# Optimization experiments

Hardware: AMD Instinct MI355X
Metric: run time of the kernel (lower is better)

The kernel has to match this reference:

```python
import jax, jax.numpy as jnp
import numpy as np

N_NODES = 100000
N_EDGES = 1600000
VOCAB = 1000
EMB = 128
HID = 256
N_GRAPHS = 128
N_LABELS = 2


def setup_inputs() -> dict:
    key = jax.random.key(0)
    ks = jax.random.split(key, 16)
    s = 0.05
    inp = {
        "x_ids": jax.random.randint(ks[0], (N_NODES,), 0, VOCAB),
        "edge_index": jax.random.randint(ks[1], (2, N_EDGES), 0, N_NODES),
        "batch": jnp.sort(jax.random.randint(ks[2], (N_NODES,), 0, N_GRAPHS)),
        "emb": jax.random.normal(ks[3], (VOCAB, EMB)) * s,
        "W0": jax.random.normal(ks[4], (EMB, HID)) * s,
        "b0": jnp.zeros((HID,)),
        "W1": jax.random.normal(ks[5], (HID, HID)) * s,
        "b1": jnp.zeros((HID,)),
        "W2": jax.random.normal(ks[6], (HID, HID)) * s,
        "b2": jnp.zeros((HID,)),
        "W3": jax.random.normal(ks[7], (HID, HID)) * s,
        "b3": jnp.zeros((HID,)),
        "Wc1": jax.random.normal(ks[8], (2 * HID, HID)) * s,
        "bc1": jnp.zeros((HID,)),
        "Wc2": jax.random.normal(ks[9], (HID, N_LABELS)) * s,
        "bc2": jnp.zeros((N_LABELS,)),
    }
    return inp


def _gcn_conv(x, W, b, src, dst, dis):
    # GCNConv with self-loops: out = D^-1/2 (A+I) D^-1/2 (x W) + b
    xw = x @ W                                   # [N, H]
    norm = dis[src] * dis[dst]                   # [E]
    out = jnp.zeros_like(xw).at[dst].add(xw[src] * norm[:, None])
    out = out + xw * (dis * dis)[:, None]        # self-loop term
    return out + b


def reference(x_ids, edge_index, batch, emb, W0, b0, W1, b1, W2, b2, W3, b3,
              Wc1, bc1, Wc2, bc2):
    src, dst = edge_index[0], edge_index[1]
    # degree (incl. self loop) is the same every layer -> compute once
    deg = jnp.zeros((N_NODES,), jnp.float32).at[dst].add(1.0) + 1.0
    dis = jax.lax.rsqrt(deg)

    x = emb[x_ids]                               # [N, EMB]
    for W, b in ((W0, b0), (W1, b1), (W2, b2), (W3, b3)):
        x = jax.nn.relu(_gcn_conv(x, W, b, src, dst, dis))
        # dropout: identity in eval mode

    counts = jax.ops.segment_sum(jnp.ones((N_NODES,), x.dtype), batch,
                                 num_segments=N_GRAPHS)
    mean_pool = jax.ops.segment_sum(x, batch, num_segments=N_GRAPHS)
    mean_pool = mean_pool / jnp.maximum(counts, 1.0)[:, None]
    max_pool = jax.ops.segment_max(x, batch, num_segments=N_GRAPHS)
    max_pool = jnp.where(counts[:, None] > 0, max_pool, 0.0)

    g = jnp.concatenate([mean_pool, max_pool], axis=1)  # [G, 2H]
    h = jax.nn.relu(g @ Wc1 + bc1)
    logits = h @ Wc2 + bc2                               # [G, 2]
    return logits
```

## Files before the change

kernel.cpp:

```cpp
#include <hip/hip_runtime.h>
#include <hip/hip_bf16.h>
#include <cstdint>
#include <cstddef>

#define N_NODES 100000
#define N_EDGES 1600000
#define EMBD 128
#define HID 256
#define N_GRAPHS 128
#define VOCAB 1000
#define NB_SCAN 98

typedef short bf16x8 __attribute__((ext_vector_type(8)));
typedef float f32x4 __attribute__((ext_vector_type(4)));
typedef float f32x2 __attribute__((ext_vector_type(2)));

__device__ inline unsigned short rne_bf16(float f) {
  unsigned u = __float_as_uint(f);
  return (unsigned short)((u + 0x7FFFu + ((u >> 16) & 1u)) >> 16);
}
__device__ inline float bf16_to_f32(unsigned short h) {
  return __uint_as_float(((unsigned)h) << 16);
}
__device__ inline void split_hl(float v, unsigned short& h, unsigned short& l) {
  h = rne_bf16(v);
  float hf = __uint_as_float(((unsigned)h) << 16);
  l = rne_bf16(v - hf);
}
__device__ inline f32x4 cvt4(uint2 v) {
  f32x4 r;
  r[0] = __uint_as_float(v.x << 16);
  r[1] = __uint_as_float(v.x & 0xFFFF0000u);
  r[2] = __uint_as_float(v.y << 16);
  r[3] = __uint_as_float(v.y & 0xFFFF0000u);
  return r;
}
__device__ inline f32x2 cvt2(unsigned v) {
  f32x2 r;
  r[0] = __uint_as_float(v << 16);
  r[1] = __uint_as_float(v & 0xFFFF0000u);
  return r;
}

__global__ void k_indeg(const int* __restrict__ dst, int* __restrict__ indeg) {
  int e = blockIdx.x * 256 + threadIdx.x;
  if (e < N_EDGES) atomicAdd(&indeg[dst[e]], 1);
}

__global__ __launch_bounds__(1024)
void k_scan1(const int* __restrict__ indeg, int* __restrict__ off, int* __restrict__ bsum,
             float* __restrict__ dis) {
  __shared__ int s[1024];
  const int tid = threadIdx.x;
  int i = blockIdx.x * 1024 + tid;
  int v = (i < N_NODES) ? indeg[i] : 0;
  if (i < N_NODES) dis[i] = rsqrtf((float)(v + 1));
  s[tid] = v; __syncthreads();
  #pragma unroll
  for (int ofs = 1; ofs < 1024; ofs <<= 1) {
    int t2 = (tid >= ofs) ? s[tid - ofs] : 0;
    __syncthreads();
    s[tid] += t2;
    __syncthreads();
  }
  if (i < N_NODES) off[i] = s[tid] - v;
  if (tid == 1023) bsum[blockIdx.x] = s[1023];
}

__global__ void k_scan2(int* __restrict__ bsum) {
  if (threadIdx.x == 0) {
    int a = 0;
    for (int i = 0; i < NB_SCAN; ++i) { int t = bsum[i]; bsum[i] = a; a += t; }
    bsum[NB_SCAN] = a;
  }
}

__global__ __launch_bounds__(1024)
void k_scan3(int* __restrict__ off, int* __restrict__ cur, const int* __restrict__ bsum) {
  int i = blockIdx.x * 1024 + threadIdx.x;
  if (i < N_NODES) { int v = off[i] + bsum[blockIdx.x]; off[i] = v; cur[i] = v; }
  if (i == 0) off[N_NODES] = bsum[NB_SCAN];
}

__global__ void k_fill(const int* __restrict__ src, const int* __restrict__ dst,
                       const int* __restrict__ ids, const float* __restrict__ dis,
                       int* __restrict__ cursor, int2* __restrict__ csre,
                       int2* __restrict__ csre0) {
  int e = blockIdx.x * 256 + threadIdx.x;
  if (e < N_EDGES) {
    int s = src[e];
    float ds = dis[s];
    int p = atomicAdd(&cursor[dst[e]], 1);
    csre[p]  = make_int2(s, __float_as_int(ds));
    csre0[p] = make_int2(ids[s], __float_as_int(ds));
  }
}

__global__ void k_prep(const float* __restrict__ emb, unsigned short* __restrict__ emb16,
                       const float* __restrict__ W0, unsigned short* __restrict__ w0h,
                       unsigned short* __restrict__ w0l,
                       const float* __restrict__ W1, unsigned short* __restrict__ w1h,
                       unsigned short* __restrict__ w1l,
                       const float* __restrict__ W2, unsigned short* __restrict__ w2h,
                       unsigned short* __restrict__ w2l,
                       const float* __restrict__ W3, unsigned short* __restrict__ w3h,
                       unsigned short* __restrict__ w3l) {
  int i = blockIdx.x * 256 + threadIdx.x;
  if (i < VOCAB * EMBD) { emb16[i] = rne_bf16(emb[i]); return; }
  i -= VOCAB * EMBD;
  unsigned short h, l;
  if (i < EMBD * HID) {
    int k = i >> 8, n = i & 255;
    split_hl(W0[i], h, l);
    w0h[n * EMBD + k] = h; w0l[n * EMBD + k] = l;
    return;
  }
  i -= EMBD * HID;
  if (i >= 3 * HID * HID) return;
  int w = i >> 16, j = i & 65535;
  const float* Ws = (w == 0) ? W1 : (w == 1) ? W2 : W3;
  unsigned short* th = (w == 0) ? w1h : (w == 1) ? w2h : w3h;
  unsigned short* tl = (w == 0) ? w1l : (w == 1) ? w2l : w3l;
  int k = j >> 8, n = j & 255;
  split_hl(Ws[j], h, l);
  th[n * HID + k] = h; tl[n * HID + k] = l;
}

__global__ __launch_bounds__(256)
void k_agg0(const unsigned short* __restrict__ emb16, const int* __restrict__ ids,
            const float* __restrict__ dis, const int* __restrict__ off,
            const int2* __restrict__ csre0, unsigned short* __restrict__ aggA) {
  const int lane = threadIdx.x & 63;
  const int node = blockIdx.x * 4 + (threadIdx.x >> 6);
  const float di = dis[node];
  unsigned sv = *((const unsigned*)(emb16 + (size_t)ids[node] * EMBD) + lane);
  f32x2 a0 = di * cvt2(sv);
  f32x2 a1 = (f32x2)0.f, a2 = (f32x2)0.f, a3 = (f32x2)0.f;
  const int e0 = off[node], e1 = off[node + 1];
  int e = e0;
  for (; e + 4 <= e1; e += 4) {
    int2 c0 = csre0[e], c1 = csre0[e + 1], c2 = csre0[e + 2], c3 = csre0[e + 3];
    unsigned v0 = *((const unsigned*)(emb16 + (size_t)c0.x * EMBD) + lane);
    unsigned v1 = *((const unsigned*)(emb16 + (size_t)c1.x * EMBD) + lane);
    unsigned v2 = *((const unsigned*)(emb16 + (size_t)c2.x * EMBD) + lane);
    unsigned v3 = *((const unsigned*)(emb16 + (size_t)c3.x * EMBD) + lane);
    a0 += __int_as_float(c0.y) * cvt2(v0);
    a1 += __int_as_float(c1.y) * cvt2(v1);
    a2 += __int_as_float(c2.y) * cvt2(v2);
    a3 += __int_as_float(c3.y) * cvt2(v3);
  }
  for (; e < e1; ++e) {
    int2 c0 = csre0[e];
    unsigned v0 = *((const unsigned*)(emb16 + (size_t)c0.x * EMBD) + lane);
    a0 += __int_as_float(c0.y) * cvt2(v0);
  }
  f32x2 r = di * ((a0 + a1) + (a2 + a3));
  size_t base = (size_t)node * EMBD + lane * 2;
  *(ushort2*)&aggA[base] = make_ushort2(rne_bf16(r[0]), rne_bf16(r[1]));
}

__global__ __launch_bounds__(256)
void k_agg16(const unsigned short* __restrict__ y16, const float* __restrict__ dis,
             const int* __restrict__ off, const int2* __restrict__ csre,
             unsigned short* __restrict__ aggA) {
  const int lane = threadIdx.x & 63;
  const int node = blockIdx.x * 4 + (threadIdx.x >> 6);
  const float di = dis[node];
  uint2 sv = *((const uint2*)(y16 + (size_t)node * HID) + lane);
  f32x4 a0 = di * cvt4(sv);
  f32x4 a1 = (f32x4)0.f, a2 = (f32x4)0.f, a3 = (f32x4)0.f;
  const int e0 = off[node], e1 = off[node + 1];
  int e = e0;
  for (; e + 4 <= e1; e += 4) {
    int2 c0 = csre[e], c1 = csre[e + 1], c2 = csre[e + 2], c3 = csre[e + 3];
    uint2 v0 = *((const uint2*)(y16 + (size_t)c0.x * HID) + lane);
    uint2 v1 = *((const uint2*)(y16 + (size_t)c1.x * HID) + lane);
    uint2 v2 = *((const uint2*)(y16 + (size_t)c2.x * HID) + lane);
    uint2 v3 = *((const uint2*)(y16 + (size_t)c3.x * HID) + lane);
    a0 += __int_as_float(c0.y) * cvt4(v0);
    a1 += __int_as_float(c1.y) * cvt4(v1);
    a2 += __int_as_float(c2.y) * cvt4(v2);
    a3 += __int_as_float(c3.y) * cvt4(v3);
  }
  for (; e < e1; ++e) {
    int2 c0 = csre[e];
    uint2 v0 = *((const uint2*)(y16 + (size_t)c0.x * HID) + lane);
    a0 += __int_as_float(c0.y) * cvt4(v0);
  }
  f32x4 r = di * ((a0 + a1) + (a2 + a3));
  size_t base = (size_t)node * HID + lane * 4;
  *(ushort4*)&aggA[base] = make_ushort4(rne_bf16(r[0]), rne_bf16(r[1]),
                                        rne_bf16(r[2]), rne_bf16(r[3]));
}

template<int K>
__global__ __launch_bounds__(256)
void k_gemm_direct(const unsigned short* __restrict__ A,
                   const unsigned short* __restrict__ Wh, const unsigned short* __restrict__ Wl,
                   const float* __restrict__ bias, unsigned short* __restrict__ C16) {
  const int lane = threadIdx.x & 63;
  const int wid = threadIdx.x >> 6;
  const int wr = wid >> 1, wc = wid & 1;
  const int row0 = blockIdx.x * 128;
  const int col0 = blockIdx.y * 128;
  const int cl = lane & 15;
  const int sl = lane >> 4;

  int ra[4];
  #pragma unroll
  for (int f = 0; f < 4; ++f) {
    int r = row0 + wr * 64 + f * 16 + cl;
    ra[f] = (r < N_NODES) ? r : (N_NODES - 1);
  }
  const int cb = col0 + wc * 64 + cl;

  f32x4 acc[4][4];
  #pragma unroll
  for (int i = 0; i < 4; ++i)
    #pragma unroll
    for (int j = 0; j < 4; ++j) acc[i][j] = (f32x4)0.f;

  #pragma unroll
  for (int kt = 0; kt < K; kt += 32) {
    bf16x8 fa[4], fbh[4], fbl[4];
    #pragma unroll
    for (int f = 0; f < 4; ++f) {
      fa[f]  = *(const bf16x8*)&A [(size_t)ra[f] * K + kt + sl * 8];
      fbh[f] = *(const bf16x8*)&Wh[(size_t)(cb + f * 16) * K + kt + sl * 8];
      fbl[f] = *(const bf16x8*)&Wl[(size_t)(cb + f * 16) * K + kt + sl * 8];
    }
    #pragma unroll
    for (int i = 0; i < 4; ++i)
      #pragma unroll
      for (int j = 0; j < 4; ++j) {
        acc[i][j] = __builtin_amdgcn_mfma_f32_16x16x32_bf16(fa[i], fbh[j], acc[i][j], 0, 0, 0);
        acc[i][j] = __builtin_amdgcn_mfma_f32_16x16x32_bf16(fa[i], fbl[j], acc[i][j], 0, 0, 0);
      }
  }

  #pragma unroll
  for (int j = 0; j < 4; ++j) {
    int gn = col0 + wc * 64 + j * 16 + cl;
    float bn = bias[gn];
    #pragma unroll
    for (int i = 0; i < 4; ++i) {
      f32x4 v = acc[i][j];
      #pragma unroll
      for (int r = 0; r < 4; ++r) {
        int gm = row0 + wr * 64 + i * 16 + sl * 4 + r;
        if (gm < N_NODES) C16[(size_t)gm * HID + gn] = rne_bf16(fmaxf(v[r] + bn, 0.f));
      }
    }
  }
}

__device__ inline int lower_bound_i(const int* a, int n, int v) {
  int lo = 0, hi = n;
  while (lo < hi) { int m = (lo + hi) >> 1; if (a[m] < v) lo = m + 1; else hi = m; }
  return lo;
}

__global__ __launch_bounds__(256)
void k_pool(const unsigned short* __restrict__ y16, const int* __restrict__ batch,
            float* __restrict__ gsum, float* __restrict__ gmax) {
  const int gi = blockIdx.x, ck = blockIdx.y, t = threadIdx.x;
  const int start = lower_bound_i(batch, N_NODES, gi);
  const int end   = lower_bound_i(batch, N_NODES, gi + 1);
  const int len = end - start;
  const int c0 = start + (len * ck) / 4;
  const int c1 = start + (len * (ck + 1)) / 4;
  float sum = 0.f, mx = 0.f;
  #pragma unroll 4
  for (int n = c0; n < c1; ++n) {
    float v = bf16_to_f32(y16[(size_t)n * HID + t]);
    sum += v; mx = fmaxf(mx, v);
  }
  if (c0 < c1) {
    atomicAdd(&gsum[gi * HID + t], sum);
    atomicMax((int*)&gmax[gi * HID + t], __float_as_int(mx));
  }
}

__global__ __launch_bounds__(256)
void k_cls(const float* __restrict__ gsum, const float* __restrict__ gmax,
           const int* __restrict__ batch,
           const float* __restrict__ Wc1, const float* __restrict__ bc1,
           const float* __restrict__ Wc2, const float* __restrict__ bc2,
           float* __restrict__ out) {
  const int gi = blockIdx.x, t = threadIdx.x;
  __shared__ float sg[512];
  __shared__ float sh[256];
  const int start = lower_bound_i(batch, N_NODES, gi);
  const int end   = lower_bound_i(batch, N_NODES, gi + 1);
  const float rcnt = 1.f / (float)((end - start) > 0 ? (end - start) : 1);
  sg[t] = gsum[gi * HID + t] * rcnt;
  sg[256 + t] = gmax[gi * HID + t];
  __syncthreads();
  float a = bc1[t];
  #pragma unroll 8
  for (int k = 0; k < 512; ++k) a = fmaf(sg[k], Wc1[k * HID + t], a);
  sh[t] = fmaxf(a, 0.f);
  __syncthreads();
  if (t < 2) {
    float o = bc2[t];
    for (int k = 0; k < 256; ++k) o = fmaf(sh[k], Wc2[k * 2 + t], o);
    out[gi * 2 + t] = o;
  }
}

extern "C" void kernel_launch(void* const* d_in, const int* in_sizes, int n_in,
                              void* d_out, int out_size, void* d_ws, size_t ws_size,
                              hipStream_t stream) {
  const int*   x_ids = (const int*)d_in[0];
  const int*   ei    = (const int*)d_in[1];
  const int*   batch = (const int*)d_in[2];
  const float* emb   = (const float*)d_in[3];
  const float* W0 = (const float*)d_in[4];  const float* b0 = (const float*)d_in[5];
  const float* W1 = (const float*)d_in[6];  const float* b1 = (const float*)d_in[7];
  const float* W2 = (const float*)d_in[8];  const float* b2 = (const float*)d_in[9];
  const float* W3 = (const float*)d_in[10]; const float* b3 = (const float*)d_in[11];
  const float* Wc1 = (const float*)d_in[12]; const float* bc1 = (const float*)d_in[13];
  const float* Wc2 = (const float*)d_in[14]; const float* bc2 = (const float*)d_in[15];
  float* out = (float*)d_out;
  const int* src = ei;
  const int* dst = ei + N_EDGES;

  char* ws = (char*)d_ws;
  size_t o = 0;
  auto alloc = [&](size_t bytes) -> char* {
    char* p = ws + o; o += (bytes + 255) & ~(size_t)255; return p;
  };
  unsigned short* y16  = (unsigned short*)alloc((size_t)N_NODES * HID * 2);
  unsigned short* aggA = (unsigned short*)alloc((size_t)N_NODES * HID * 2);
  float* dis   = (float*)alloc((size_t)N_NODES * 4);
  int*   indeg = (int*)  alloc((size_t)N_NODES * 4);
  int*   off   = (int*)  alloc((size_t)(N_NODES + 1) * 4);
  int*   cur   = (int*)  alloc((size_t)(N_NODES + 1) * 4);
  int*   bsum  = (int*)  alloc((size_t)(NB_SCAN + 1) * 4);
  int2*  csre  = (int2*) alloc((size_t)N_EDGES * 8);
  int2*  csre0 = (int2*) alloc((size_t)N_EDGES * 8);
  unsigned short* emb16 = (unsigned short*)alloc((size_t)VOCAB * EMBD * 2);
  unsigned short* wbuf  = (unsigned short*)alloc((size_t)458752 * 2);
  float* gsum  = (float*)alloc((size_t)N_GRAPHS * HID * 4);
  float* gmax  = (float*)alloc((size_t)N_GRAPHS * HID * 4);
  (void)ws_size; (void)in_sizes; (void)n_in; (void)out_size;

  unsigned short* wt0h = wbuf;            unsigned short* wt0l = wbuf + 32768;
  unsigned short* wt1h = wbuf + 65536;    unsigned short* wt1l = wbuf + 131072;
  unsigned short* wt2h = wbuf + 196608;   unsigned short* wt2l = wbuf + 262144;
  unsigned short* wt3h = wbuf + 327680;   unsigned short* wt3l = wbuf + 393216;

  hipMemsetAsync(indeg, 0, (size_t)N_NODES * 4, stream);
  hipMemsetAsync(gsum, 0, (size_t)N_GRAPHS * HID * 4 * 2, stream);
  k_indeg<<<N_EDGES / 256, 256, 0, stream>>>(dst, indeg);
  k_scan1<<<NB_SCAN, 1024, 0, stream>>>(indeg, off, bsum, dis);
  k_scan2<<<1, 64, 0, stream>>>(bsum);
  k_scan3<<<NB_SCAN, 1024, 0, stream>>>(off, cur, bsum);
  k_fill<<<N_EDGES / 256, 256, 0, stream>>>(src, dst, x_ids, dis, cur, csre, csre0);
  k_prep<<<(VOCAB * EMBD + EMBD * HID + 3 * HID * HID + 255) / 256, 256, 0, stream>>>(
      emb, emb16, W0, wt0h, wt0l, W1, wt1h, wt1l, W2, wt2h, wt2l, W3, wt3h, wt3l);

  dim3 ggrid((N_NODES + 127) / 128, 2);
  k_agg0<<<N_NODES / 4, 256, 0, stream>>>(emb16, x_ids, dis, off, csre0, aggA);
  k_gemm_direct<128><<<ggrid, 256, 0, stream>>>(aggA, wt0h, wt0l, b0, y16);
  k_agg16<<<N_NODES / 4, 256, 0, stream>>>(y16, dis, off, csre, aggA);
  k_gemm_direct<256><<<ggrid, 256, 0, stream>>>(aggA, wt1h, wt1l, b1, y16);
  k_agg16<<<N_NODES / 4, 256, 0, stream>>>(y16, dis, off, csre, aggA);
  k_gemm_direct<256><<<ggrid, 256, 0, stream>>>(aggA, wt2h, wt2l, b2, y16);
  k_agg16<<<N_NODES / 4, 256, 0, stream>>>(y16, dis, off, csre, aggA);
  k_gemm_direct<256><<<ggrid, 256, 0, stream>>>(aggA, wt3h, wt3l, b3, y16);

  dim3 pgrid(N_GRAPHS, 4);
  k_pool<<<pgrid, 256, 0, stream>>>(y16, batch, gsum, gmax);
  k_cls<<<N_GRAPHS, 256, 0, stream>>>(gsum, gmax, batch, Wc1, bc1, Wc2, bc2, out);
}
```

Before: 1.079 ms.

## Fuse GCN neighbor aggregation into the GEMM via shared-memory row tiles

Each layer now runs one kernel: a block aggregates 64 node rows from the CSR into LDS as bf16, then does the split-bf16 MFMA GEMM across all 256 output columns with bias and ReLU, ping-ponging between two output buffers. This removes the global write and re-read of the aggregated activation matrix and halves kernel launches. In exchange each block runs its gather phase before its compute phase with only 4 waves, and the GEMM no longer tiles columns across blocks. The block-sum scan is also parallelised across 128 threads.

Result: slower. 1.289 ms (+19.4%).

```diff
diff --git a/kernel.cpp b/kernel.cpp
--- a/kernel.cpp
+++ b/kernel.cpp
@@ -68,11 +68,19 @@
 }
 
 __global__ void k_scan2(int* __restrict__ bsum) {
-  if (threadIdx.x == 0) {
-    int a = 0;
-    for (int i = 0; i < NB_SCAN; ++i) { int t = bsum[i]; bsum[i] = a; a += t; }
-    bsum[NB_SCAN] = a;
-  }
+  __shared__ int s[128];
+  const int t = threadIdx.x;
+  int v = (t < NB_SCAN) ? bsum[t] : 0;
+  s[t] = v; __syncthreads();
+  #pragma unroll
+  for (int ofs = 1; ofs < 128; ofs <<= 1) {
+    int x = (t >= ofs) ? s[t - ofs] : 0;
+    __syncthreads();
+    s[t] += x;
+    __syncthreads();
+  }
+  if (t < NB_SCAN) bsum[t] = s[t] - v;
+  if (t == 127) bsum[NB_SCAN] = s[127];
 }
 
 __global__ __launch_bounds__(1024)
@@ -126,108 +134,102 @@
   th[n * HID + k] = h; tl[n * HID + k] = l;
 }
 
-__global__ __launch_bounds__(256)
-void k_agg0(const unsigned short* __restrict__ emb16, const int* __restrict__ ids,
-            const float* __restrict__ dis, const int* __restrict__ off,
-            const int2* __restrict__ csre0, unsigned short* __restrict__ aggA) {
-  const int lane = threadIdx.x & 63;
-  const int node = blockIdx.x * 4 + (threadIdx.x >> 6);
-  const float di = dis[node];
-  unsigned sv = *((const unsigned*)(emb16 + (size_t)ids[node] * EMBD) + lane);
-  f32x2 a0 = di * cvt2(sv);
-  f32x2 a1 = (f32x2)0.f, a2 = (f32x2)0.f, a3 = (f32x2)0.f;
-  const int e0 = off[node], e1 = off[node + 1];
-  int e = e0;
-  for (; e + 4 <= e1; e += 4) {
-    int2 c0 = csre0[e], c1 = csre0[e + 1], c2 = csre0[e + 2], c3 = csre0[e + 3];
-    unsigned v0 = *((const unsigned*)(emb16 + (size_t)c0.x * EMBD) + lane);
-    unsigned v1 = *((const unsigned*)(emb16 + (size_t)c1.x * EMBD) + lane);
-    unsigned v2 = *((const unsigned*)(emb16 + (size_t)c2.x * EMBD) + lane);
-    unsigned v3 = *((const unsigned*)(emb16 + (size_t)c3.x * EMBD) + lane);
-    a0 += __int_as_float(c0.y) * cvt2(v0);
-    a1 += __int_as_float(c1.y) * cvt2(v1);
-    a2 += __int_as_float(c2.y) * cvt2(v2);
-    a3 += __int_as_float(c3.y) * cvt2(v3);
-  }
-  for (; e < e1; ++e) {
-    int2 c0 = csre0[e];
-    unsigned v0 = *((const unsigned*)(emb16 + (size_t)c0.x * EMBD) + lane);
-    a0 += __int_as_float(c0.y) * cvt2(v0);
-  }
-  f32x2 r = di * ((a0 + a1) + (a2 + a3));
-  size_t base = (size_t)node * EMBD + lane * 2;
-  *(ushort2*)&aggA[base] = make_ushort2(rne_bf16(r[0]), rne_bf16(r[1]));
-}
-
-__global__ __launch_bounds__(256)
-void k_agg16(const unsigned short* __restrict__ y16, const float* __restrict__ dis,
-             const int* __restrict__ off, const int2* __restrict__ csre,
-             unsigned short* __restrict__ aggA) {
-  const int lane = threadIdx.x & 63;
-  const int node = blockIdx.x * 4 + (threadIdx.x >> 6);
-  const float di = dis[node];
-  uint2 sv = *((const uint2*)(y16 + (size_t)node * HID) + lane);
-  f32x4 a0 = di * cvt4(sv);
-  f32x4 a1 = (f32x4)0.f, a2 = (f32x4)0.f, a3 = (f32x4)0.f;
-  const int e0 = off[node], e1 = off[node + 1];
-  int e = e0;
-  for (; e + 4 <= e1; e += 4) {
-    int2 c0 = csre[e], c1 = csre[e + 1], c2 = csre[e + 2], c3 = csre[e + 3];
-    uint2 v0 = *((const uint2*)(y16 + (size_t)c0.x * HID) + lane);
-    uint2 v1 = *((const uint2*)(y16 + (size_t)c1.x * HID) + lane);
-    uint2 v2 = *((const uint2*)(y16 + (size_t)c2.x * HID) + lane);
-    uint2 v3 = *((const uint2*)(y16 + (size_t)c3.x * HID) + lane);
-    a0 += __int_as_float(c0.y) * cvt4(v0);
-    a1 += __int_as_float(c1.y) * cvt4(v1);
-    a2 += __int_as_float(c2.y) * cvt4(v2);
-    a3 += __int_as_float(c3.y) * cvt4(v3);
-  }
-  for (; e < e1; ++e) {
-    int2 c0 = csre[e];
-    uint2 v0 = *((const uint2*)(y16 + (size_t)c0.x * HID) + lane);
-    a0 += __int_as_float(c0.y) * cvt4(v0);
-  }
-  f32x4 r = di * ((a0 + a1) + (a2 + a3));
-  size_t base = (size_t)node * HID + lane * 4;
-  *(ushort4*)&aggA[base] = make_ushort4(rne_bf16(r[0]), rne_bf16(r[1]),
-                                        rne_bf16(r[2]), rne_bf16(r[3]));
-}
-
 template<int K>
 __global__ __launch_bounds__(256)
-void k_gemm_direct(const unsigned short* __restrict__ A,
-                   const unsigned short* __restrict__ Wh, const unsigned short* __restrict__ Wl,
-                   const float* __restrict__ bias, unsigned short* __restrict__ C16) {
-  const int lane = threadIdx.x & 63;
-  const int wid = threadIdx.x >> 6;
-  const int wr = wid >> 1, wc = wid & 1;
-  const int row0 = blockIdx.x * 128;
-  const int col0 = blockIdx.y * 128;
+void k_fused(const unsigned short* __restrict__ xin, const int* __restrict__ ids,
+             const float* __restrict__ dis, const int* __restrict__ off,
+             const int2* __restrict__ csre,
+             const unsigned short* __restrict__ Wh, const unsigned short* __restrict__ Wl,
+             const float* __restrict__ bias, unsigned short* __restrict__ yout) {
+  constexpr int LDA = K + 8;
+  __shared__ unsigned short sA[64 * LDA];
+  const int tid = threadIdx.x;
+  const int lane = tid & 63;
+  const int wid = tid >> 6;
+  const int row0 = blockIdx.x * 64;
+
+  for (int n = 0; n < 16; ++n) {
+    const int lrow = wid * 16 + n;
+    const int node = row0 + lrow;
+    if constexpr (K == 256) {
+      f32x4 a0 = (f32x4)0.f, a1 = (f32x4)0.f, a2 = (f32x4)0.f, a3 = (f32x4)0.f;
+      if (node < N_NODES) {
+        const float di = dis[node];
+        uint2 sv = *((const uint2*)(xin + (size_t)node * 256) + lane);
+        a0 = di * cvt4(sv);
+        const int e0 = off[node], e1 = off[node + 1];
+        int e = e0;
+        for (; e + 4 <= e1; e += 4) {
+          int2 c0 = csre[e], c1 = csre[e + 1], c2 = csre[e + 2], c3 = csre[e + 3];
+          uint2 v0 = *((const uint2*)(xin + (size_t)c0.x * 256) + lane);
+          uint2 v1 = *((const uint2*)(xin + (size_t)c1.x * 256) + lane);
+          uint2 v2 = *((const uint2*)(xin + (size_t)c2.x * 256) + lane);
+          uint2 v3 = *((const uint2*)(xin + (size_t)c3.x * 256) + lane);
+          a0 += __int_as_float(c0.y) * cvt4(v0);
+          a1 += __int_as_float(c1.y) * cvt4(v1);
+          a2 += __int_as_float(c2.y) * cvt4(v2);
+          a3 += __int_as_float(c3.y) * cvt4(v3);
+        }
+        for (; e < e1; ++e) {
+          int2 c0 = csre[e];
+          uint2 v0 = *((const uint2*)(xin + (size_t)c0.x * 256) + lane);
+          a0 += __int_as_float(c0.y) * cvt4(v0);
+        }
+        f32x4 r = di * ((a0 + a1) + (a2 + a3));
+        *(ushort4*)&sA[lrow * LDA + lane * 4] =
+            make_ushort4(rne_bf16(r[0]), rne_bf16(r[1]), rne_bf16(r[2]), rne_bf16(r[3]));
+      } else {
+        *(ushort4*)&sA[lrow * LDA + lane * 4] = make_ushort4(0, 0, 0, 0);
+      }
+    } else {
+      f32x2 a0 = (f32x2)0.f, a1 = (f32x2)0.f, a2 = (f32x2)0.f, a3 = (f32x2)0.f;
+      if (node < N_NODES) {
+        const float di = dis[node];
+        unsigned sv = *((const unsigned*)(xin + (size_t)ids[node] * 128) + lane);
+        a0 = di * cvt2(sv);
+        const int e0 = off[node], e1 = off[node + 1];
+        int e = e0;
+        for (; e + 4 <= e1; e += 4) {
+          int2 c0 = csre[e], c1 = csre[e + 1], c2 = csre[e + 2], c3 = csre[e + 3];
+          unsigned v0 = *((const unsigned*)(xin + (size_t)c0.x * 128) + lane);
+          unsigned v1 = *((const unsigned*)(xin + (size_t)c1.x * 128) + lane);
+          unsigned v2 = *((const unsigned*)(xin + (size_t)c2.x * 128) + lane);
+          unsigned v3 = *((const unsigned*)(xin + (size_t)c3.x * 128) + lane);
+          a0 += __int_as_float(c0.y) * cvt2(v0);
+          a1 += __int_as_float(c1.y) * cvt2(v1);
+          a2 += __int_as_float(c2.y) * cvt2(v2);
+          a3 += __int_as_float(c3.y) * cvt2(v3);
+        }
+        for (; e < e1; ++e) {
+          int2 c0 = csre[e];
+          unsigned v0 = *((const unsigned*)(xin + (size_t)c0.x * 128) + lane);
+          a0 += __int_as_float(c0.y) * cvt2(v0);
+        }
+        f32x2 r = di * ((a0 + a1) + (a2 + a3));
+        *(ushort2*)&sA[lrow * LDA + lane * 2] = make_ushort2(rne_bf16(r[0]), rne_bf16(r[1]));
+      } else {
+        *(ushort2*)&sA[lrow * LDA + lane * 2] = make_ushort2(0, 0);
+      }
+    }
+  }
+  __syncthreads();
+
   const int cl = lane & 15;
   const int sl = lane >> 4;
-
-  int ra[4];
-  #pragma unroll
-  for (int f = 0; f < 4; ++f) {
-    int r = row0 + wr * 64 + f * 16 + cl;
-    ra[f] = (r < N_NODES) ? r : (N_NODES - 1);
-  }
-  const int cb = col0 + wc * 64 + cl;
-
   f32x4 acc[4][4];
   #pragma unroll
   for (int i = 0; i < 4; ++i)
     #pragma unroll
     for (int j = 0; j < 4; ++j) acc[i][j] = (f32x4)0.f;
 
-  #pragma unroll
   for (int kt = 0; kt < K; kt += 32) {
     bf16x8 fa[4], fbh[4], fbl[4];
     #pragma unroll
     for (int f = 0; f < 4; ++f) {
-      fa[f]  = *(const bf16x8*)&A [(size_t)ra[f] * K + kt + sl * 8];
-      fbh[f] = *(const bf16x8*)&Wh[(size_t)(cb + f * 16) * K + kt + sl * 8];
-      fbl[f] = *(const bf16x8*)&Wl[(size_t)(cb + f * 16) * K + kt + sl * 8];
+      fa[f]  = *(const bf16x8*)&sA[(f * 16 + cl) * LDA + kt + sl * 8];
+      int wrow = wid * 64 + f * 16 + cl;
+      fbh[f] = *(const bf16x8*)&Wh[(size_t)wrow * K + kt + sl * 8];
+      fbl[f] = *(const bf16x8*)&Wl[(size_t)wrow * K + kt + sl * 8];
     }
     #pragma unroll
     for (int i = 0; i < 4; ++i)
@@ -240,15 +242,15 @@
 
   #pragma unroll
   for (int j = 0; j < 4; ++j) {
-    int gn = col0 + wc * 64 + j * 16 + cl;
+    int gn = wid * 64 + j * 16 + cl;
     float bn = bias[gn];
     #pragma unroll
     for (int i = 0; i < 4; ++i) {
       f32x4 v = acc[i][j];
       #pragma unroll
       for (int r = 0; r < 4; ++r) {
-        int gm = row0 + wr * 64 + i * 16 + sl * 4 + r;
-        if (gm < N_NODES) C16[(size_t)gm * HID + gn] = rne_bf16(fmaxf(v[r] + bn, 0.f));
+        int gm = row0 + i * 16 + sl * 4 + r;
+        if (gm < N_NODES) yout[(size_t)gm * HID + gn] = rne_bf16(fmaxf(v[r] + bn, 0.f));
       }
     }
   }
@@ -330,8 +332,8 @@
   auto alloc = [&](size_t bytes) -> char* {
     char* p = ws + o; o += (bytes + 255) & ~(size_t)255; return p;
   };
-  unsigned short* y16  = (unsigned short*)alloc((size_t)N_NODES * HID * 2);
-  unsigned short* aggA = (unsigned short*)alloc((size_t)N_NODES * HID * 2);
+  unsigned short* yA   = (unsigned short*)alloc((size_t)N_NODES * HID * 2);
+  unsigned short* yB   = (unsigned short*)alloc((size_t)N_NODES * HID * 2);
   float* dis   = (float*)alloc((size_t)N_NODES * 4);
   int*   indeg = (int*)  alloc((size_t)N_NODES * 4);
   int*   off   = (int*)  alloc((size_t)(N_NODES + 1) * 4);
@@ -354,23 +356,19 @@
   hipMemsetAsync(gsum, 0, (size_t)N_GRAPHS * HID * 4 * 2, stream);
   k_indeg<<<N_EDGES / 256, 256, 0, stream>>>(dst, indeg);
   k_scan1<<<NB_SCAN, 1024, 0, stream>>>(indeg, off, bsum, dis);
-  k_scan2<<<1, 64, 0, stream>>>(bsum);
+  k_scan2<<<1, 128, 0, stream>>>(bsum);
   k_scan3<<<NB_SCAN, 1024, 0, stream>>>(off, cur, bsum);
   k_fill<<<N_EDGES / 256, 256, 0, stream>>>(src, dst, x_ids, dis, cur, csre, csre0);
   k_prep<<<(VOCAB * EMBD + EMBD * HID + 3 * HID * HID + 255) / 256, 256, 0, stream>>>(
       emb, emb16, W0, wt0h, wt0l, W1, wt1h, wt1l, W2, wt2h, wt2l, W3, wt3h, wt3l);
 
-  dim3 ggrid((N_NODES + 127) / 128, 2);
-  k_agg0<<<N_NODES / 4, 256, 0, stream>>>(emb16, x_ids, dis, off, csre0, aggA);
-  k_gemm_direct<128><<<ggrid, 256, 0, stream>>>(aggA, wt0h, wt0l, b0, y16);
-  k_agg16<<<N_NODES / 4, 256, 0, stream>>>(y16, dis, off, csre, aggA);
-  k_gemm_direct<256><<<ggrid, 256, 0, stream>>>(aggA, wt1h, wt1l, b1, y16);
-  k_agg16<<<N_NODES / 4, 256, 0, stream>>>(y16, dis, off, csre, aggA);
-  k_gemm_direct<256><<<ggrid, 256, 0, stream>>>(aggA, wt2h, wt2l, b2, y16);
-  k_agg16<<<N_NODES / 4, 256, 0, stream>>>(y16, dis, off, csre, aggA);
-  k_gemm_direct<256><<<ggrid, 256, 0, stream>>>(aggA, wt3h, wt3l, b3, y16);
+  const int nblk = (N_NODES + 63) / 64;
+  k_fused<128><<<nblk, 256, 0, stream>>>(emb16, x_ids, dis, off, csre0, wt0h, wt0l, b0, yA);
+  k_fused<256><<<nblk, 256, 0, stream>>>(yA, nullptr, dis, off, csre, wt1h, wt1l, b1, yB);
+  k_fused<256><<<nblk, 256, 0, stream>>>(yB, nullptr, dis, off, csre, wt2h, wt2l, b2, yA);
+  k_fused<256><<<nblk, 256, 0, stream>>>(yA, nullptr, dis, off, csre, wt3h, wt3l, b3, yB);
 
   dim3 pgrid(N_GRAPHS, 4);
-  k_pool<<<pgrid, 256, 0, stream>>>(y16, batch, gsum, gmax);
+  k_pool<<<pgrid, 256, 0, stream>>>(yB, batch, gsum, gmax);
   k_cls<<<N_GRAPHS, 256, 0, stream>>>(gsum, gmax, batch, Wc1, bc1, Wc2, bc2, out);
 }
```
